# Performance work log

Hardware: AMD Instinct MI355X
Metric: run time of the kernel (lower is better)

## Reference

```python
import jax, jax.numpy as jnp
import numpy as np

NEG = -1.0e30  # stand-in for -inf, safe under logaddexp in fp32
DEN_SCALE = 1.0


def _ctc_forward(logp, targets, in_lens, tgt_lens):
    """Log-semiring forward (tot score) over the numerator lattice:
    CTC topology composed with the linear target FSA. logp: [B,T,C] (blank=0),
    targets: [B,U] in [1, C-1]. Returns [B] numerator log-scores."""
    B, T, C = logp.shape
    U = targets.shape[1]
    S = 2 * U + 1  # extended label sequence: blank-interleaved
    ext = jnp.zeros((B, S), dtype=jnp.int32).at[:, 1::2].set(targets.astype(jnp.int32))
    # skip transition s-2 -> s allowed only for non-blank, non-repeated labels
    skip_ok = jnp.concatenate(
        [jnp.zeros((B, 2), dtype=bool), (ext[:, 2:] != 0) & (ext[:, 2:] != ext[:, :-2])],
        axis=1,
    )
    emit0 = jnp.take_along_axis(logp[:, 0], ext, axis=1)  # [B,S]
    alpha = jnp.full((B, S), NEG, dtype=logp.dtype)
    alpha = alpha.at[:, 0].set(emit0[:, 0]).at[:, 1].set(emit0[:, 1])
    logp_t = jnp.swapaxes(logp, 0, 1)  # [T,B,C]

    def step(alpha, xs):
        t, lp = xs
        a1 = jnp.concatenate([jnp.full((B, 1), NEG, alpha.dtype), alpha[:, :-1]], axis=1)
        a2 = jnp.concatenate([jnp.full((B, 2), NEG, alpha.dtype), alpha[:, :-2]], axis=1)
        cand = jnp.logaddexp(jnp.logaddexp(alpha, a1), jnp.where(skip_ok, a2, NEG))
        new = cand + jnp.take_along_axis(lp, ext, axis=1)
        alpha = jnp.where((t < in_lens)[:, None], new, alpha)  # freeze past utterance end
        return alpha, None

    alpha, _ = jax.lax.scan(step, alpha, (jnp.arange(1, T), logp_t[1:]))
    last = (2 * tgt_lens).astype(jnp.int32)  # final states: last blank / last label
    a_last = jnp.take_along_axis(alpha, last[:, None], axis=1)[:, 0]
    a_prev = jnp.take_along_axis(alpha, (last - 1)[:, None], axis=1)[:, 0]
    return jnp.logaddexp(a_last, a_prev)


def _den_forward(logp, trans, start, in_lens):
    """Log-semiring forward over the dense denominator graph (bigram token LM):
    states = token classes, transition log-weights trans[C,C]. Returns [B]."""
    B, T, C = logp.shape
    alpha = start[None, :] + logp[:, 0]  # [B,C]
    logp_t = jnp.swapaxes(logp, 0, 1)  # [T,B,C]

    def step(alpha, xs):
        t, lp = xs
        new = jax.nn.logsumexp(alpha[:, :, None] + trans[None], axis=1) + lp
        alpha = jnp.where((t < in_lens)[:, None], new, alpha)
        return alpha, None

    alpha, _ = jax.lax.scan(step, alpha, (jnp.arange(1, T), logp_t[1:]))
    return jax.nn.logsumexp(alpha, axis=1)


def setup_inputs() -> dict:
    key = jax.random.key(0)
    ks = jax.random.split(key, 6)
    B, T, C, U = 32, 2000, 256, 200
    log_probs = jax.nn.log_softmax(jax.random.normal(ks[0], (B, T, C), dtype=jnp.float32), axis=-1)
    targets = jax.random.randint(ks[1], (B, U), 1, C)
    input_lengths = jax.random.randint(ks[2], (B,), T // 2, T + 1)
    target_lengths = jax.random.randint(ks[3], (B,), U // 2, U + 1)
    den_transitions = jax.random.normal(ks[4], (C, C), dtype=jnp.float32) * 0.1
    den_start = jax.random.normal(ks[5], (C,), dtype=jnp.float32) * 0.1
    return {
        "log_probs": log_probs,
        "targets": targets,
        "input_lengths": input_lengths,
        "target_lengths": target_lengths,
        "den_transitions": den_transitions,
        "den_start": den_start,
    }


def reference(log_probs, targets, input_lengths, target_lengths, den_transitions, den_start):
    logp = jax.nn.log_softmax(log_probs, axis=-1)  # idempotent if already normalized
    B, T, C = logp.shape
    U = targets.shape[1]
    in_lens = jnp.clip(input_lengths, 2 * U + 1, T).astype(jnp.int32)
    tgt_lens = jnp.clip(target_lengths, 1, U).astype(jnp.int32)
    tgt = jnp.clip(targets, 1, C - 1)  # blank=0 excluded from targets
    num = _ctc_forward(logp, tgt, in_lens, tgt_lens)
    den = _den_forward(logp, den_transitions, den_start, in_lens)
    tot = num - DEN_SCALE * den  # LF-MMI per-utterance objective
    valid = tot > 0.5 * NEG  # mimic get_tot_objf_and_num_frames -inf filtering
    n = jnp.maximum(jnp.sum(valid), 1)
    return -jnp.sum(jnp.where(valid, tot, 0.0)) / n
```

## Files before the change

kernel.cpp:

```cpp
#include <hip/hip_runtime.h>
#include <stdint.h>
#include <stddef.h>

#define NEGF (-1.0e30f)

typedef __attribute__((ext_vector_type(2))) _Float16 half2_t;
typedef uint32_t u32x16 __attribute__((ext_vector_type(16)));

constexpr int Bn = 32;
constexpr int Tn = 2000;
constexpr int Cn = 256;
constexpr int Un = 200;
constexpr int Sn = 2 * Un + 1;
constexpr float Kn = 4096.0f;

__device__ __forceinline__ float fdot2f(uint32_t a, uint32_t b, float c) {
  half2_t ha = __builtin_bit_cast(half2_t, a);
  half2_t hb = __builtin_bit_cast(half2_t, b);
#if __has_builtin(__builtin_amdgcn_fdot2)
  return __builtin_amdgcn_fdot2(ha, hb, c, false);
#else
  return c + (float)ha.x * (float)hb.x + (float)ha.y * (float)hb.y;
#endif
}

template <int CTRL>
__device__ __forceinline__ float dppf(float x) {
#if __has_builtin(__builtin_amdgcn_update_dpp)
  int xi = __builtin_bit_cast(int, x);
  int y = __builtin_amdgcn_update_dpp(0, xi, CTRL, 0xF, 0xF, false);
  return __builtin_bit_cast(float, y);
#else
  return x;
#endif
}
#define dpp_x1(v) dppf<0xB1>(v)
#define dpp_x2(v) dppf<0x4E>(v)
#define dpp_x7(v) dppf<0x141>(v)

__device__ __forceinline__ uint32_t packe(float a, float b) {
  half2_t h;
  h.x = (_Float16)a;
  h.y = (_Float16)b;
  return __builtin_bit_cast(uint32_t, h);
}

__device__ __forceinline__ float lse3(float a, float b, float c) {
  float m = fmaxf(fmaxf(a, b), c);
  return m + __logf(__expf(a - m) + __expf(b - m) + __expf(c - m));
}

__device__ __forceinline__ int clampi(int v, int lo, int hi) {
  return v < lo ? lo : (v > hi ? hi : v);
}

__device__ __forceinline__ void barrier_nodrain() {
  asm volatile("s_waitcnt lgkmcnt(0)" ::: "memory");
  __builtin_amdgcn_s_barrier();
  asm volatile("" ::: "memory");
}

__global__ __launch_bounds__(256)
__attribute__((amdgpu_waves_per_eu(1, 1)))
void fwd_kernel(
    const float* __restrict__ logp, const int* __restrict__ targets,
    const int* __restrict__ in_lens, const int* __restrict__ tgt_lens,
    const float* __restrict__ trans, const float* __restrict__ start,
    float* __restrict__ ws) {
  const int tid = threadIdx.x;
  const int bid = blockIdx.x;

  if (bid < Bn) {
    const int b = bid;
    const int L = clampi(in_lens[b], Sn, Tn);
    const int q = tid & 7;
    const int u = tid >> 3;
    const int jw = u + 32 * q;

    __shared__ __align__(16) char eaLDS[2 * 8 * 80];
    __shared__ float sred[4];

    const float* trow = trans;
#define EP(c, m) packe(__expf(trow[(32 * q + 2 * (m)) * Cn + (c)]), \
                       __expf(trow[(32 * q + 2 * (m) + 1) * Cn + (c)]))
#define MKCOL(c)                                                          \
  (u32x16){EP(c, 0),  EP(c, 1),  EP(c, 2),  EP(c, 3),  EP(c, 4),          \
           EP(c, 5),  EP(c, 6),  EP(c, 7),  EP(c, 8),  EP(c, 9),          \
           EP(c, 10), EP(c, 11), EP(c, 12), EP(c, 13), EP(c, 14), EP(c, 15)}
    u32x16 E0 = MKCOL(u + 0);
    u32x16 E1 = MKCOL(u + 32);
    u32x16 E2 = MKCOL(u + 64);
    u32x16 E3 = MKCOL(u + 96);
    u32x16 E4 = MKCOL(u + 128);
    u32x16 E5 = MKCOL(u + 160);
    u32x16 E6 = MKCOL(u + 192);
    u32x16 E7 = MKCOL(u + 224);
#undef MKCOL
#undef EP

    const float* lpb = logp + (size_t)b * Tn * Cn;
    const char* rbase0 = eaLDS + 80 * q;
    char* wptr0 = eaLDS + 80 * q + 2 * u;

    float G = -__logf(Kn);
    *(_Float16*)(wptr0) = (_Float16)(Kn * __expf(start[jw] + lpb[jw]));
    float lp0 = lpb[Cn + jw];
    float lp1 = lpb[(size_t)2 * Cn + jw];
    __syncthreads();

    const uint32_t ONE2 = 0x3C003C00u;
    const bool q4 = (q & 4) != 0, q2 = (q & 2) != 0, q1 = (q & 1) != 0;

    for (int t = 1; t < L; ++t) {
      const int pr = (t - 1) & 1, pw = t & 1;
      const float lp_cur = lp0;
      lp0 = lp1;
      const int tpre = (t + 2 < L) ? t + 2 : L - 1;
      lp1 = lpb[(size_t)tpre * Cn + jw];
      const float p = __expf(lp_cur);

      const uint4* eap = (const uint4*)(rbase0 + pr * 640);
      float a0 = 0.f, a1 = 0.f, a2 = 0.f, a3 = 0.f;
      float a4 = 0.f, a5 = 0.f, a6 = 0.f, a7 = 0.f;
      half2_t zpk = {(_Float16)0.f, (_Float16)0.f};
#define B2(x) __builtin_bit_cast(half2_t, x)
#define DOT8(idx, ev)               \
  a0 = fdot2f(E0[idx], ev, a0);     \
  a1 = fdot2f(E1[idx], ev, a1);     \
  a2 = fdot2f(E2[idx], ev, a2);     \
  a3 = fdot2f(E3[idx], ev, a3);     \
  a4 = fdot2f(E4[idx], ev, a4);     \
  a5 = fdot2f(E5[idx], ev, a5);     \
  a6 = fdot2f(E6[idx], ev, a6);     \
  a7 = fdot2f(E7[idx], ev, a7);
#define DOTQ(m4)                                                      \
  {                                                                   \
    const uint4 e4 = eap[m4];                                         \
    DOT8(4 * (m4) + 0, e4.x)                                          \
    DOT8(4 * (m4) + 1, e4.y)                                          \
    DOT8(4 * (m4) + 2, e4.z)                                          \
    DOT8(4 * (m4) + 3, e4.w)                                          \
    zpk = zpk + ((B2(e4.x) + B2(e4.y)) + (B2(e4.z) + B2(e4.w)));      \
  }
      DOTQ(0)
      DOTQ(1)
      DOTQ(2)
      DOTQ(3)
#undef DOTQ
#undef DOT8

      float zc = fdot2f(ONE2, __builtin_bit_cast(uint32_t, zpk), 0.f);
      zc += dpp_x1(zc);
      zc += dpp_x2(zc);
      zc += dpp_x7(zc);

      float g, t0, t1, t2, t3, w0, w1, s;
      g = q4 ? a0 : a4;  t0 = (q4 ? a4 : a0) + dpp_x7(g);
      g = q4 ? a1 : a5;  t1 = (q4 ? a5 : a1) + dpp_x7(g);
      g = q4 ? a2 : a6;  t2 = (q4 ? a6 : a2) + dpp_x7(g);
      g = q4 ? a3 : a7;  t3 = (q4 ? a7 : a3) + dpp_x7(g);
      g = q2 ? t0 : t2;  w0 = (q2 ? t2 : t0) + dpp_x2(g);
      g = q2 ? t1 : t3;  w1 = (q2 ? t3 : t1) + dpp_x2(g);
      g = q1 ? w0 : w1;  s  = (q1 ? w1 : w0) + dpp_x1(g);

      const float invZ = Kn * __frcp_rn(zc);
      G -= __logf(invZ);
      *(_Float16*)(wptr0 + pw * 640) = (_Float16)(s * p * invZ);
      barrier_nodrain();
    }

    {
      const int pL = (L - 1) & 1;
      const char* fb = eaLDS + pL * 640;
      float e = (float)(*(const _Float16*)(fb + 80 * (tid >> 5) + 2 * (tid & 31)));
#pragma unroll
      for (int off = 32; off >= 1; off >>= 1) e += __shfl_xor(e, off, 64);
      const int lane = tid & 63, wid = tid >> 6;
      if (lane == 0) sred[wid] = e;
      __syncthreads();
      if (tid == 0) {
        float ssum = (sred[0] + sred[1]) + (sred[2] + sred[3]);
        ws[Bn + b] = G + __logf(ssum);
      }
    }
  } else {
    const int b = bid - Bn;
    const int L = clampi(in_lens[b], Sn, Tn);
    const int tl = clampi(tgt_lens[b], 1, Un);

    __shared__ float abuf[2][Sn + 3];
    const float* lpb = logp + (size_t)b * Tn * Cn;
    const int* tgtb = targets + b * Un;

    const int s1 = tid;
    const int s2 = tid + 256;
    int e1 = 0, e2 = 0;
    bool k1 = false, k2 = false;
    if (s1 & 1) {
      const int uu = (s1 - 1) >> 1;
      e1 = clampi(tgtb[uu], 1, Cn - 1);
      if (uu > 0) k1 = (e1 != clampi(tgtb[uu - 1], 1, Cn - 1));
    }
    if ((s2 < Sn) && (s2 & 1)) {
      const int uu = (s2 - 1) >> 1;
      e2 = clampi(tgtb[uu], 1, Cn - 1);
      k2 = (e2 != clampi(tgtb[uu - 1], 1, Cn - 1));
    }

    abuf[0][s1 + 2] = (s1 == 0) ? lpb[0] : (s1 == 1 ? lpb[e1] : NEGF);
    if (s2 < Sn) abuf[0][s2 + 2] = NEGF;
    if (tid < 2) { abuf[0][tid] = NEGF; abuf[1][tid] = NEGF; }
    float pe1_0 = lpb[Cn + e1];
    float pe2_0 = lpb[Cn + e2];
    float pe1_1 = lpb[(size_t)2 * Cn + e1];
    float pe2_1 = lpb[(size_t)2 * Cn + e2];
    __syncthreads();

    int cur = 0;
    for (int t = 1; t < L; ++t) {
      const float em1 = pe1_0, em2 = pe2_0;
      pe1_0 = pe1_1;
      pe2_0 = pe2_1;
      const int tpre = (t + 2 < L) ? t + 2 : L - 1;
      pe1_1 = lpb[(size_t)tpre * Cn + e1];
      pe2_1 = lpb[(size_t)tpre * Cn + e2];
      const float* A = abuf[cur];
      float* Bv = abuf[cur ^ 1];
      {
        const float x = A[s1 + 2], y = A[s1 + 1];
        const float z = k1 ? A[s1] : NEGF;
        Bv[s1 + 2] = lse3(x, y, z) + em1;
      }
      if (s2 < Sn) {
        const float x = A[s2 + 2], y = A[s2 + 1];
        const float z = k2 ? A[s2] : NEGF;
        Bv[s2 + 2] = lse3(x, y, z) + em2;
      }
      barrier_nodrain();
      cur ^= 1;
    }
    if (tid == 0) {
      const int l = 2 * tl;
      const float x = abuf[cur][l + 2], y = abuf[cur][l + 1];
      const float m = fmaxf(x, y);
      ws[b] = m + __logf(__expf(x - m) + __expf(y - m));
    }
  }
}

__global__ void finalize_kernel(const float* __restrict__ ws,
                                float* __restrict__ out) {
  const int tid = threadIdx.x;
  float tot = 0.f, cnt = 0.f;
  if (tid < Bn) {
    const float tv = ws[tid] - ws[Bn + tid];
    const bool valid = tv > 0.5f * NEGF;
    tot = valid ? tv : 0.f;
    cnt = valid ? 1.f : 0.f;
  }
#pragma unroll
  for (int off = 32; off >= 1; off >>= 1) {
    tot += __shfl_xor(tot, off, 64);
    cnt += __shfl_xor(cnt, off, 64);
  }
  if (tid == 0) out[0] = -tot / fmaxf(cnt, 1.f);
}

extern "C" void kernel_launch(void* const* d_in, const int* in_sizes, int n_in,
                              void* d_out, int out_size, void* d_ws, size_t ws_size,
                              hipStream_t stream) {
  const float* logp = (const float*)d_in[0];
  const int* targets = (const int*)d_in[1];
  const int* in_lens = (const int*)d_in[2];
  const int* tgt_lens = (const int*)d_in[3];
  const float* trans = (const float*)d_in[4];
  const float* start = (const float*)d_in[5];
  float* ws = (float*)d_ws;
  float* out = (float*)d_out;
  (void)in_sizes; (void)n_in; (void)out_size; (void)ws_size;

  fwd_kernel<<<dim3(2 * Bn), dim3(256), 0, stream>>>(
      logp, targets, in_lens, tgt_lens, trans, start, ws);
  finalize_kernel<<<dim3(1), dim3(64), 0, stream>>>(ws, out);
}
```

Measured before the change: 1.046 ms.

## Process two utterances per workgroup to share barriers and latency

Each workgroup now runs the recursion for two batch elements at once, in both the denominator and numerator branches, halving the grid from 64 to 32 blocks. The two independent dot-product and logsumexp chains are interleaved within one step and share a single barrier, so their latency can overlap. Per-utterance length masking freezes finished sequences, and the loop runs to the larger of the two lengths. The cost is more work per step on each CU, and the loop length is set by the longer utterance of each pair.

```diff
diff --git a/kernel.cpp b/kernel.cpp
--- a/kernel.cpp
+++ b/kernel.cpp
@@ -60,6 +60,7 @@
   asm volatile("" ::: "memory");
 }
 
+
 __global__ __launch_bounds__(256)
 __attribute__((amdgpu_waves_per_eu(1, 1)))
 void fwd_kernel(
@@ -70,15 +71,17 @@
   const int tid = threadIdx.x;
   const int bid = blockIdx.x;
 
-  if (bid < Bn) {
-    const int b = bid;
-    const int L = clampi(in_lens[b], Sn, Tn);
+  if (bid < 16) {
+    const int bA = 2 * bid, bB = bA + 1;
+    const int LA = clampi(in_lens[bA], Sn, Tn);
+    const int LB = clampi(in_lens[bB], Sn, Tn);
+    const int Lm = LA > LB ? LA : LB;
     const int q = tid & 7;
     const int u = tid >> 3;
     const int jw = u + 32 * q;
 
-    __shared__ __align__(16) char eaLDS[2 * 8 * 80];
-    __shared__ float sred[4];
+    __shared__ __align__(16) char eaLDS[2 * 1280];
+    __shared__ float sredA[4], sredB[4];
 
     const float* trow = trans;
 #define EP(c, m) packe(__expf(trow[(32 * q + 2 * (m)) * Cn + (c)]), \
@@ -98,33 +101,44 @@
 #undef MKCOL
 #undef EP
 
-    const float* lpb = logp + (size_t)b * Tn * Cn;
-    const char* rbase0 = eaLDS + 80 * q;
-    char* wptr0 = eaLDS + 80 * q + 2 * u;
-
-    float G = -__logf(Kn);
-    *(_Float16*)(wptr0) = (_Float16)(Kn * __expf(start[jw] + lpb[jw]));
-    float lp0 = lpb[Cn + jw];
-    float lp1 = lpb[(size_t)2 * Cn + jw];
+    const float* lpA = logp + (size_t)bA * Tn * Cn;
+    const float* lpB = logp + (size_t)bB * Tn * Cn;
+    const char* rbA = eaLDS + 80 * q;
+    const char* rbB = eaLDS + 1280 + 80 * q;
+    char* wpA = eaLDS + 80 * q + 2 * u;
+    char* wpB = eaLDS + 1280 + 80 * q + 2 * u;
+
+    float GA = -__logf(Kn), GB = -__logf(Kn);
+    _Float16 pvA = (_Float16)(Kn * __expf(start[jw] + lpA[jw]));
+    _Float16 pvB = (_Float16)(Kn * __expf(start[jw] + lpB[jw]));
+    *(_Float16*)wpA = pvA;
+    *(_Float16*)wpB = pvB;
+    float lpA0 = lpA[Cn + jw], lpA1 = lpA[(size_t)2 * Cn + jw];
+    float lpB0 = lpB[Cn + jw], lpB1 = lpB[(size_t)2 * Cn + jw];
     __syncthreads();
 
     const uint32_t ONE2 = 0x3C003C00u;
     const bool q4 = (q & 4) != 0, q2 = (q & 2) != 0, q1 = (q & 1) != 0;
 
-    for (int t = 1; t < L; ++t) {
+    for (int t = 1; t < Lm; ++t) {
       const int pr = (t - 1) & 1, pw = t & 1;
-      const float lp_cur = lp0;
-      lp0 = lp1;
-      const int tpre = (t + 2 < L) ? t + 2 : L - 1;
-      lp1 = lpb[(size_t)tpre * Cn + jw];
-      const float p = __expf(lp_cur);
-
-      const uint4* eap = (const uint4*)(rbase0 + pr * 640);
+      const float pA = __expf(lpA0), pB = __expf(lpB0);
+      lpA0 = lpA1;
+      lpB0 = lpB1;
+      const int tpre = (t + 2 < Lm) ? t + 2 : Lm - 1;
+      lpA1 = lpA[(size_t)tpre * Cn + jw];
+      lpB1 = lpB[(size_t)tpre * Cn + jw];
+
+      const uint4* eapA = (const uint4*)(rbA + pr * 640);
+      const uint4* eapB = (const uint4*)(rbB + pr * 640);
       float a0 = 0.f, a1 = 0.f, a2 = 0.f, a3 = 0.f;
       float a4 = 0.f, a5 = 0.f, a6 = 0.f, a7 = 0.f;
-      half2_t zpk = {(_Float16)0.f, (_Float16)0.f};
+      float c0 = 0.f, c1 = 0.f, c2 = 0.f, c3 = 0.f;
+      float c4 = 0.f, c5 = 0.f, c6 = 0.f, c7 = 0.f;
+      half2_t zpA = {(_Float16)0.f, (_Float16)0.f};
+      half2_t zpB = {(_Float16)0.f, (_Float16)0.f};
 #define B2(x) __builtin_bit_cast(half2_t, x)
-#define DOT8(idx, ev)               \
+#define DOT8A(idx, ev)              \
   a0 = fdot2f(E0[idx], ev, a0);     \
   a1 = fdot2f(E1[idx], ev, a1);     \
   a2 = fdot2f(E2[idx], ev, a2);     \
@@ -133,117 +147,217 @@
   a5 = fdot2f(E5[idx], ev, a5);     \
   a6 = fdot2f(E6[idx], ev, a6);     \
   a7 = fdot2f(E7[idx], ev, a7);
-#define DOTQ(m4)                                                      \
+#define DOT8B(idx, ev)              \
+  c0 = fdot2f(E0[idx], ev, c0);     \
+  c1 = fdot2f(E1[idx], ev, c1);     \
+  c2 = fdot2f(E2[idx], ev, c2);     \
+  c3 = fdot2f(E3[idx], ev, c3);     \
+  c4 = fdot2f(E4[idx], ev, c4);     \
+  c5 = fdot2f(E5[idx], ev, c5);     \
+  c6 = fdot2f(E6[idx], ev, c6);     \
+  c7 = fdot2f(E7[idx], ev, c7);
+#define DOTQA(m4)                                                     \
   {                                                                   \
-    const uint4 e4 = eap[m4];                                         \
-    DOT8(4 * (m4) + 0, e4.x)                                          \
-    DOT8(4 * (m4) + 1, e4.y)                                          \
-    DOT8(4 * (m4) + 2, e4.z)                                          \
-    DOT8(4 * (m4) + 3, e4.w)                                          \
-    zpk = zpk + ((B2(e4.x) + B2(e4.y)) + (B2(e4.z) + B2(e4.w)));      \
-  }
-      DOTQ(0)
-      DOTQ(1)
-      DOTQ(2)
-      DOTQ(3)
-#undef DOTQ
-#undef DOT8
-
-      float zc = fdot2f(ONE2, __builtin_bit_cast(uint32_t, zpk), 0.f);
-      zc += dpp_x1(zc);
-      zc += dpp_x2(zc);
-      zc += dpp_x7(zc);
-
-      float g, t0, t1, t2, t3, w0, w1, s;
+    const uint4 e4 = eapA[m4];                                        \
+    DOT8A(4 * (m4) + 0, e4.x)                                         \
+    DOT8A(4 * (m4) + 1, e4.y)                                         \
+    DOT8A(4 * (m4) + 2, e4.z)                                         \
+    DOT8A(4 * (m4) + 3, e4.w)                                         \
+    zpA = zpA + ((B2(e4.x) + B2(e4.y)) + (B2(e4.z) + B2(e4.w)));      \
+  }
+#define DOTQB(m4)                                                     \
+  {                                                                   \
+    const uint4 e4 = eapB[m4];                                        \
+    DOT8B(4 * (m4) + 0, e4.x)                                         \
+    DOT8B(4 * (m4) + 1, e4.y)                                         \
+    DOT8B(4 * (m4) + 2, e4.z)                                         \
+    DOT8B(4 * (m4) + 3, e4.w)                                         \
+    zpB = zpB + ((B2(e4.x) + B2(e4.y)) + (B2(e4.z) + B2(e4.w)));      \
+  }
+      DOTQA(0)
+      DOTQB(0)
+      DOTQA(1)
+      DOTQB(1)
+      DOTQA(2)
+      DOTQB(2)
+      DOTQA(3)
+      DOTQB(3)
+#undef DOTQA
+#undef DOTQB
+#undef DOT8A
+#undef DOT8B
+#undef B2
+
+      float zcA = fdot2f(ONE2, __builtin_bit_cast(uint32_t, zpA), 0.f);
+      float zcB = fdot2f(ONE2, __builtin_bit_cast(uint32_t, zpB), 0.f);
+      zcA += dpp_x1(zcA);
+      zcB += dpp_x1(zcB);
+      zcA += dpp_x2(zcA);
+      zcB += dpp_x2(zcB);
+      zcA += dpp_x7(zcA);
+      zcB += dpp_x7(zcB);
+
+      float g, t0, t1, t2, t3, w0, w1, sA, sB;
       g = q4 ? a0 : a4;  t0 = (q4 ? a4 : a0) + dpp_x7(g);
       g = q4 ? a1 : a5;  t1 = (q4 ? a5 : a1) + dpp_x7(g);
       g = q4 ? a2 : a6;  t2 = (q4 ? a6 : a2) + dpp_x7(g);
       g = q4 ? a3 : a7;  t3 = (q4 ? a7 : a3) + dpp_x7(g);
       g = q2 ? t0 : t2;  w0 = (q2 ? t2 : t0) + dpp_x2(g);
       g = q2 ? t1 : t3;  w1 = (q2 ? t3 : t1) + dpp_x2(g);
-      g = q1 ? w0 : w1;  s  = (q1 ? w1 : w0) + dpp_x1(g);
-
-      const float invZ = Kn * __frcp_rn(zc);
-      G -= __logf(invZ);
-      *(_Float16*)(wptr0 + pw * 640) = (_Float16)(s * p * invZ);
+      g = q1 ? w0 : w1;  sA = (q1 ? w1 : w0) + dpp_x1(g);
+      g = q4 ? c0 : c4;  t0 = (q4 ? c4 : c0) + dpp_x7(g);
+      g = q4 ? c1 : c5;  t1 = (q4 ? c5 : c1) + dpp_x7(g);
+      g = q4 ? c2 : c6;  t2 = (q4 ? c6 : c2) + dpp_x7(g);
+      g = q4 ? c3 : c7;  t3 = (q4 ? c7 : c3) + dpp_x7(g);
+      g = q2 ? t0 : t2;  w0 = (q2 ? t2 : t0) + dpp_x2(g);
+      g = q2 ? t1 : t3;  w1 = (q2 ? t3 : t1) + dpp_x2(g);
+      g = q1 ? w0 : w1;  sB = (q1 ? w1 : w0) + dpp_x1(g);
+
+      const float invZA = Kn * __frcp_rn(zcA);
+      const float invZB = Kn * __frcp_rn(zcB);
+      if (t < LA) {
+        GA -= __logf(invZA);
+        pvA = (_Float16)(sA * pA * invZA);
+      }
+      if (t < LB) {
+        GB -= __logf(invZB);
+        pvB = (_Float16)(sB * pB * invZB);
+      }
+      *(_Float16*)(wpA + pw * 640) = pvA;
+      *(_Float16*)(wpB + pw * 640) = pvB;
       barrier_nodrain();
     }
 
     {
-      const int pL = (L - 1) & 1;
-      const char* fb = eaLDS + pL * 640;
-      float e = (float)(*(const _Float16*)(fb + 80 * (tid >> 5) + 2 * (tid & 31)));
+      const int pL = (Lm - 1) & 1;
+      const char* fA = eaLDS + pL * 640;
+      const char* fB = eaLDS + 1280 + pL * 640;
+      float eA = (float)(*(const _Float16*)(fA + 80 * (tid >> 5) + 2 * (tid & 31)));
+      float eB = (float)(*(const _Float16*)(fB + 80 * (tid >> 5) + 2 * (tid & 31)));
 #pragma unroll
-      for (int off = 32; off >= 1; off >>= 1) e += __shfl_xor(e, off, 64);
+      for (int off = 32; off >= 1; off >>= 1) {
+        eA += __shfl_xor(eA, off, 64);
+        eB += __shfl_xor(eB, off, 64);
+      }
       const int lane = tid & 63, wid = tid >> 6;
-      if (lane == 0) sred[wid] = e;
+      if (lane == 0) {
+        sredA[wid] = eA;
+        sredB[wid] = eB;
+      }
       __syncthreads();
       if (tid == 0) {
-        float ssum = (sred[0] + sred[1]) + (sred[2] + sred[3]);
-        ws[Bn + b] = G + __logf(ssum);
+        ws[Bn + bA] = GA + __logf((sredA[0] + sredA[1]) + (sredA[2] + sredA[3]));
+        ws[Bn + bB] = GB + __logf((sredB[0] + sredB[1]) + (sredB[2] + sredB[3]));
       }
     }
   } else {
-    const int b = bid - Bn;
-    const int L = clampi(in_lens[b], Sn, Tn);
-    const int tl = clampi(tgt_lens[b], 1, Un);
-
-    __shared__ float abuf[2][Sn + 3];
-    const float* lpb = logp + (size_t)b * Tn * Cn;
-    const int* tgtb = targets + b * Un;
+    const int nb = bid - 16;
+    const int bA = 2 * nb, bB = bA + 1;
+    const int LA = clampi(in_lens[bA], Sn, Tn);
+    const int LB = clampi(in_lens[bB], Sn, Tn);
+    const int Lm = LA > LB ? LA : LB;
+
+    __shared__ float abuf[2][2][Sn + 3];
+    const float* lpA = logp + (size_t)bA * Tn * Cn;
+    const float* lpB = logp + (size_t)bB * Tn * Cn;
+    const int* tgA = targets + bA * Un;
+    const int* tgB = targets + bB * Un;
 
     const int s1 = tid;
     const int s2 = tid + 256;
-    int e1 = 0, e2 = 0;
-    bool k1 = false, k2 = false;
+    int e1A = 0, e2A = 0, e1B = 0, e2B = 0;
+    bool k1A = false, k2A = false, k1B = false, k2B = false;
     if (s1 & 1) {
       const int uu = (s1 - 1) >> 1;
-      e1 = clampi(tgtb[uu], 1, Cn - 1);
-      if (uu > 0) k1 = (e1 != clampi(tgtb[uu - 1], 1, Cn - 1));
+      e1A = clampi(tgA[uu], 1, Cn - 1);
+      e1B = clampi(tgB[uu], 1, Cn - 1);
+      if (uu > 0) {
+        k1A = (e1A != clampi(tgA[uu - 1], 1, Cn - 1));
+        k1B = (e1B != clampi(tgB[uu - 1], 1, Cn - 1));
+      }
     }
     if ((s2 < Sn) && (s2 & 1)) {
       const int uu = (s2 - 1) >> 1;
-      e2 = clampi(tgtb[uu], 1, Cn - 1);
-      k2 = (e2 != clampi(tgtb[uu - 1], 1, Cn - 1));
-    }
-
-    abuf[0][s1 + 2] = (s1 == 0) ? lpb[0] : (s1 == 1 ? lpb[e1] : NEGF);
-    if (s2 < Sn) abuf[0][s2 + 2] = NEGF;
-    if (tid < 2) { abuf[0][tid] = NEGF; abuf[1][tid] = NEGF; }
-    float pe1_0 = lpb[Cn + e1];
-    float pe2_0 = lpb[Cn + e2];
-    float pe1_1 = lpb[(size_t)2 * Cn + e1];
-    float pe2_1 = lpb[(size_t)2 * Cn + e2];
+      e2A = clampi(tgA[uu], 1, Cn - 1);
+      e2B = clampi(tgB[uu], 1, Cn - 1);
+      k2A = (e2A != clampi(tgA[uu - 1], 1, Cn - 1));
+      k2B = (e2B != clampi(tgB[uu - 1], 1, Cn - 1));
+    }
+
+    abuf[0][0][s1 + 2] = (s1 == 0) ? lpA[0] : (s1 == 1 ? lpA[e1A] : NEGF);
+    abuf[0][1][s1 + 2] = (s1 == 0) ? lpB[0] : (s1 == 1 ? lpB[e1B] : NEGF);
+    if (s2 < Sn) {
+      abuf[0][0][s2 + 2] = NEGF;
+      abuf[0][1][s2 + 2] = NEGF;
+    }
+    if (tid < 2) {
+      abuf[0][0][tid] = NEGF;
+      abuf[1][0][tid] = NEGF;
+      abuf[0][1][tid] = NEGF;
+      abuf[1][1][tid] = NEGF;
+    }
+    float pe1A0 = lpA[Cn + e1A], pe2A0 = lpA[Cn + e2A];
+    float pe1B0 = lpB[Cn + e1B], pe2B0 = lpB[Cn + e2B];
+    float pe1A1 = lpA[(size_t)2 * Cn + e1A], pe2A1 = lpA[(size_t)2 * Cn + e2A];
+    float pe1B1 = lpB[(size_t)2 * Cn + e1B], pe2B1 = lpB[(size_t)2 * Cn + e2B];
     __syncthreads();
 
     int cur = 0;
-    for (int t = 1; t < L; ++t) {
-      const float em1 = pe1_0, em2 = pe2_0;
-      pe1_0 = pe1_1;
-      pe2_0 = pe2_1;
-      const int tpre = (t + 2 < L) ? t + 2 : L - 1;
-      pe1_1 = lpb[(size_t)tpre * Cn + e1];
-      pe2_1 = lpb[(size_t)tpre * Cn + e2];
-      const float* A = abuf[cur];
-      float* Bv = abuf[cur ^ 1];
+    for (int t = 1; t < Lm; ++t) {
+      const float em1A = pe1A0, em2A = pe2A0, em1B = pe1B0, em2B = pe2B0;
+      pe1A0 = pe1A1;
+      pe2A0 = pe2A1;
+      pe1B0 = pe1B1;
+      pe2B0 = pe2B1;
+      const int tpre = (t + 2 < Lm) ? t + 2 : Lm - 1;
+      pe1A1 = lpA[(size_t)tpre * Cn + e1A];
+      pe2A1 = lpA[(size_t)tpre * Cn + e2A];
+      pe1B1 = lpB[(size_t)tpre * Cn + e1B];
+      pe2B1 = lpB[(size_t)tpre * Cn + e2B];
+
+      const float* AA = abuf[cur][0];
+      const float* AB = abuf[cur][1];
+      float* BvA = abuf[cur ^ 1][0];
+      float* BvB = abuf[cur ^ 1][1];
+      const bool liveA = (t < LA), liveB = (t < LB);
       {
-        const float x = A[s1 + 2], y = A[s1 + 1];
-        const float z = k1 ? A[s1] : NEGF;
-        Bv[s1 + 2] = lse3(x, y, z) + em1;
+        const float xA = AA[s1 + 2], yA = AA[s1 + 1];
+        const float zA = k1A ? AA[s1] : NEGF;
+        const float xB = AB[s1 + 2], yB = AB[s1 + 1];
+        const float zB = k1B ? AB[s1] : NEGF;
+        const float nvA = lse3(xA, yA, zA) + em1A;
+        const float nvB = lse3(xB, yB, zB) + em1B;
+        BvA[s1 + 2] = liveA ? nvA : xA;
+        BvB[s1 + 2] = liveB ? nvB : xB;
       }
       if (s2 < Sn) {
-        const float x = A[s2 + 2], y = A[s2 + 1];
-        const float z = k2 ? A[s2] : NEGF;
-        Bv[s2 + 2] = lse3(x, y, z) + em2;
+        const float xA = AA[s2 + 2], yA = AA[s2 + 1];
+        const float zA = k2A ? AA[s2] : NEGF;
+        const float xB = AB[s2 + 2], yB = AB[s2 + 1];
+        const float zB = k2B ? AB[s2] : NEGF;
+        const float nvA = lse3(xA, yA, zA) + em2A;
+        const float nvB = lse3(xB, yB, zB) + em2B;
+        BvA[s2 + 2] = liveA ? nvA : xA;
+        BvB[s2 + 2] = liveB ? nvB : xB;
       }
       barrier_nodrain();
       cur ^= 1;
     }
     if (tid == 0) {
-      const int l = 2 * tl;
-      const float x = abuf[cur][l + 2], y = abuf[cur][l + 1];
-      const float m = fmaxf(x, y);
-      ws[b] = m + __logf(__expf(x - m) + __expf(y - m));
+      {
+        const int tl = clampi(tgt_lens[bA], 1, Un);
+        const int l = 2 * tl;
+        const float x = abuf[cur][0][l + 2], y = abuf[cur][0][l + 1];
+        const float m = fmaxf(x, y);
+        ws[bA] = m + __logf(__expf(x - m) + __expf(y - m));
+      }
+      {
+        const int tl = clampi(tgt_lens[bB], 1, Un);
+        const int l = 2 * tl;
+        const float x = abuf[cur][1][l + 2], y = abuf[cur][1][l + 1];
+        const float m = fmaxf(x, y);
+        ws[bB] = m + __logf(__expf(x - m) + __expf(y - m));
+      }
     }
   }
 }
@@ -279,7 +393,7 @@
   float* out = (float*)d_out;
   (void)in_sizes; (void)n_in; (void)out_size; (void)ws_size;
 
-  fwd_kernel<<<dim3(2 * Bn), dim3(256), 0, stream>>>(
+  fwd_kernel<<<dim3(32), dim3(256), 0, stream>>>(
       logp, targets, in_lens, tgt_lens, trans, start, ws);
   finalize_kernel<<<dim3(1), dim3(64), 0, stream>>>(ws, out);
 }
```

Measured after the change: 1.883 ms. +80.0%, slower.
